# Kernel tuning notes

Hardware: AMD Instinct MI355X
Metric: run time of the kernel (lower is better)

## Reference

```python
import jax, jax.numpy as jnp
import numpy as np

L = 4        # num_blocks
D = 512      # d_model
H = 8        # num_heads
DFF = 2048   # d_ff
EPS = 1.1920929e-07  # torch RMSNorm default eps = finfo(fp32).eps


def setup_inputs() -> dict:
    key = jax.random.key(0)
    ks = jax.random.split(key, 12)
    B, S = 4, 1024
    s = 0.02
    return {
        "x": jax.random.normal(ks[0], (B, S, D), jnp.float32),
        "col_ids": jax.random.randint(ks[1], (B, S), 0, 32),
        "row_ids": jax.random.randint(ks[2], (B, S), 0, 128),
        "nbr_ids": jax.random.randint(ks[3], (B, S), 0, 64),
        # per-block, per-relation attention weights (nn.Linear: y = x @ W.T)
        "Wq": jax.random.normal(ks[4], (L, 4, D, D), jnp.float32) * s,
        "Wk": jax.random.normal(ks[5], (L, 4, D, D), jnp.float32) * s,
        "Wv": jax.random.normal(ks[6], (L, 4, D, D), jnp.float32) * s,
        "Wo": jax.random.normal(ks[7], (L, 4, D, D), jnp.float32) * s,
        # SwiGLU FFN weights per block
        "W1": jax.random.normal(ks[8], (L, DFF, D), jnp.float32) * s,
        "W3": jax.random.normal(ks[9], (L, DFF, D), jnp.float32) * s,
        "W2": jax.random.normal(ks[10], (L, D, DFF), jnp.float32) * s,
        # RMSNorm scales: 4 attn norms + 1 ffn norm per block + final norm_out
        "g_attn": jnp.ones((L, 4, D), jnp.float32),
        "g_ffn": jnp.ones((L, D), jnp.float32),
        "g_out": jnp.ones((D,), jnp.float32),
    }


def _rms(x, g):
    return x * jax.lax.rsqrt(jnp.mean(x * x, axis=-1, keepdims=True) + EPS) * g


def _attn(x, wq, wk, wv, wo, mask):
    # x: [B,S,D]; mask: [B,S,S] bool (True = attend) or None for full attention
    B, S, _ = x.shape
    hd = D // H
    scale = 1.0 / np.sqrt(hd).astype(np.float32)
    q = (x @ wq.T).reshape(B, S, H, hd).transpose(0, 2, 1, 3)  # bhsd
    k = (x @ wk.T).reshape(B, S, H, hd).transpose(0, 2, 1, 3)
    v = (x @ wv.T).reshape(B, S, H, hd).transpose(0, 2, 1, 3)
    sc = jnp.einsum('bhqd,bhkd->bhqk', q, k) * scale
    if mask is not None:
        sc = jnp.where(mask[:, None, :, :], sc, jnp.float32(-1e30))
    a = jax.nn.softmax(sc, axis=-1)
    o = jnp.einsum('bhqk,bhkd->bhqd', a, v).transpose(0, 2, 1, 3).reshape(B, S, D)
    return o @ wo.T


def reference(x, col_ids, row_ids, nbr_ids, Wq, Wk, Wv, Wo, W1, W3, W2, g_attn, g_ffn, g_out):
    # relation order in RelationalBlock: col, feat, nbr, full
    masks = [ids[:, :, None] == ids[:, None, :] for ids in (col_ids, row_ids, nbr_ids)] + [None]
    for l in range(L):
        for r in range(4):
            x = x + _attn(_rms(x, g_attn[l, r]), Wq[l, r], Wk[l, r], Wv[l, r], Wo[l, r], masks[r])
        h = _rms(x, g_ffn[l])
        x = x + (jax.nn.silu(h @ W1[l].T) * (h @ W3[l].T)) @ W2[l].T
    return _rms(x, g_out)
```

## Files before the change

kernel.cpp:

```cpp
#include <hip/hip_runtime.h>
#include <hip/hip_bf16.h>


typedef __attribute__((ext_vector_type(4))) float f32x4;
typedef __attribute__((ext_vector_type(8))) short s16x8;
typedef __attribute__((ext_vector_type(4))) short s16x4;
typedef __attribute__((ext_vector_type(16))) short s16x16;

#define SEQ 1024
#define DM 512
#define MTOT 4096
#define EPSV 1.1920929e-07f
#define LOG2E 1.44269504088896f

static __device__ __forceinline__ float b2f(short s) {
  unsigned u = ((unsigned)(unsigned short)s) << 16;
  return __builtin_bit_cast(float, u);
}
static __device__ __forceinline__ short f2b(float f) {
  unsigned u = __builtin_bit_cast(unsigned, f);
  u = (u + 0x7fffu + ((u >> 16) & 1u)) >> 16;
  return (short)(unsigned short)u;
}

#define MFMA_BF16(a, b, c) __builtin_amdgcn_mfma_f32_16x16x32_bf16((a), (b), (c), 0, 0, 0)
#define GLLDS(gp, lp)                                                                        \
  __builtin_amdgcn_global_load_lds((const __attribute__((address_space(1))) unsigned*)(gp),  \
                                   (__attribute__((address_space(3))) unsigned*)(lp), 16, 0, 0)
#define GLLDS4(gp, lp)                                                                       \
  __builtin_amdgcn_global_load_lds((const __attribute__((address_space(1))) unsigned*)(gp),  \
                                   (__attribute__((address_space(3))) unsigned*)(lp), 4, 0, 0)

__global__ void cvt_all(const f32x4* __restrict__ wq, const f32x4* __restrict__ wk,
                        const f32x4* __restrict__ wv, const f32x4* __restrict__ wo,
                        const f32x4* __restrict__ w1, const f32x4* __restrict__ w3,
                        const f32x4* __restrict__ w2, const float* __restrict__ g_attn,
                        const float* __restrict__ g_ffn, short* __restrict__ wqkv,
                        short* __restrict__ wob, short* __restrict__ w13,
                        short* __restrict__ w2b) {
  int i0 = (blockIdx.x * 256 + threadIdx.x) * 4;
  int which = blockIdx.y;
  s16x16 o;
  if (which < 3) {
    const f32x4* src = which == 0 ? wq : (which == 1 ? wk : wv);
    f32x4 v[4];
#pragma unroll
    for (int c = 0; c < 4; c++) v[c] = src[i0 + c];
    int lr = i0 >> 16, k4 = i0 & 127, n = (i0 >> 7) & 511;
    const float* gp = g_attn + lr * 512 + k4 * 4;
    float sc = (which == 0) ? 0.125f * LOG2E : 1.0f;
#pragma unroll
    for (int c = 0; c < 4; c++)
#pragma unroll
      for (int j = 0; j < 4; j++) o[c * 4 + j] = f2b(v[c][j] * gp[c * 4 + j] * sc);
    *(s16x16*)(wqkv + ((size_t)lr * 196608 + (which * 512 + n) * 128 + k4) * 4) = o;
  } else if (which == 3 || which == 6) {
    const f32x4* src = which == 3 ? wo : w2;
    short* dst = which == 3 ? wob : w2b;
    f32x4 v[4];
#pragma unroll
    for (int c = 0; c < 4; c++) v[c] = src[i0 + c];
#pragma unroll
    for (int c = 0; c < 4; c++)
#pragma unroll
      for (int j = 0; j < 4; j++) o[c * 4 + j] = f2b(v[c][j]);
    *(s16x16*)(dst + (size_t)i0 * 4) = o;
  } else {
    const f32x4* src = which == 4 ? w1 : w3;
    int off = which - 4;
    f32x4 v[4];
#pragma unroll
    for (int c = 0; c < 4; c++) v[c] = src[i0 + c];
    int l = i0 >> 18, n = (i0 >> 7) & 2047, k4 = i0 & 127;
    const float* gp = g_ffn + l * 512 + k4 * 4;
#pragma unroll
    for (int c = 0; c < 4; c++)
#pragma unroll
      for (int j = 0; j < 4; j++) o[c * 4 + j] = f2b(v[c][j] * gp[c * 4 + j]);
    *(s16x16*)(w13 + ((size_t)l * 524288 + (n * 2 + off) * 128 + k4) * 4) = o;
  }
}

__global__ void init_kernel(const float* __restrict__ xin, float* __restrict__ x,
                            short* __restrict__ h, float* __restrict__ sbuf) {
  int gid = blockIdx.x * 256 + threadIdx.x;
  if (gid < 20 * 4096) sbuf[4096 + gid] = 0.f;
  int row = blockIdx.x * 4 + (threadIdx.x >> 6);
  int lane = threadIdx.x & 63;
  const float* xr = xin + (size_t)row * DM + lane * 8;
  f32x4 a = *(const f32x4*)xr;
  f32x4 b = *(const f32x4*)(xr + 4);
  float* xo = x + (size_t)row * DM + lane * 8;
  *(f32x4*)xo = a;
  *(f32x4*)(xo + 4) = b;
  s16x8 ho;
#pragma unroll
  for (int j = 0; j < 4; j++) { ho[j] = f2b(a[j]); ho[4 + j] = f2b(b[j]); }
  *(s16x8*)(h + (size_t)row * DM + lane * 8) = ho;
  float ss = a[0]*a[0]+a[1]*a[1]+a[2]*a[2]+a[3]*a[3]+b[0]*b[0]+b[1]*b[1]+b[2]*b[2]+b[3]*b[3];
#pragma unroll
  for (int m = 1; m < 64; m <<= 1) ss += __shfl_xor(ss, m, 64);
  if (lane == 0) sbuf[row] = ss;
}

__global__ void rmsnorm_out(const float* __restrict__ x, const float* __restrict__ g,
                            float* __restrict__ outp) {
  int row = blockIdx.x * 4 + (threadIdx.x >> 6);
  int lane = threadIdx.x & 63;
  const float* xr = x + (size_t)row * DM + lane * 8;
  f32x4 a = *(const f32x4*)xr;
  f32x4 b = *(const f32x4*)(xr + 4);
  float ss = a[0]*a[0]+a[1]*a[1]+a[2]*a[2]+a[3]*a[3]+b[0]*b[0]+b[1]*b[1]+b[2]*b[2]+b[3]*b[3];
#pragma unroll
  for (int m = 1; m < 64; m <<= 1) ss += __shfl_xor(ss, m, 64);
  float sc = rsqrtf(ss * (1.0f / DM) + EPSV);
  const float* gp = g + lane * 8;
  float* o = outp + (size_t)row * DM + lane * 8;
  f32x4 o0, o1;
#pragma unroll
  for (int j = 0; j < 4; j++) { o0[j] = a[j] * sc * gp[j]; o1[j] = b[j] * sc * gp[4 + j]; }
  *(f32x4*)o = o0;
  *(f32x4*)(o + 4) = o1;
}

template<int AR, int AC, int FUSE>
__global__ __launch_bounds__(256) void gemm_bt(const short* __restrict__ A, const short* __restrict__ W,
                                               short* __restrict__ outb, float* __restrict__ outf,
                                               short* __restrict__ vtb,
                                               const float* __restrict__ ssq_in,
                                               float* __restrict__ ssq_out,
                                               short* __restrict__ hb, int N, int K) {
  constexpr int BM = AR * 32;
  constexpr int BN = AC * 32;
  constexpr int NA = BM / 64, NB = BN / 64;
  constexpr int LPS = NA + NB;
  __shared__ short As[2][BM * 32];
  __shared__ short Bs[2][BN * 32];
  const int tid = threadIdx.x;
  const int lane = tid & 63;
  const int w = tid >> 6;
  const int wr = w >> 1, wc = w & 1;
  const int qi = lane & 15, g = lane >> 4;
  const int m0 = blockIdx.x * BM, n0 = blockIdx.y * BN;

  const short* ap[NA];
  const short* wp[NB];
#pragma unroll
  for (int i = 0; i < NA; i++) {
    int s = i * 256 + tid;
    int row = s >> 2, gl = s & 3, gd = gl ^ ((row >> 1) & 3);
    ap[i] = A + (size_t)(m0 + row) * K + gd * 8;
  }
#pragma unroll
  for (int i = 0; i < NB; i++) {
    int s = i * 256 + tid;
    int row = s >> 2, gl = s & 3, gd = gl ^ ((row >> 1) & 3);
    wp[i] = W + (size_t)(n0 + row) * K + gd * 8;
  }
  int aro[AR], bro[AC];
#pragma unroll
  for (int i = 0; i < AR; i++) {
    int row = wr * AR * 16 + i * 16 + qi;
    aro[i] = row * 64 + ((g ^ ((row >> 1) & 3)) * 16);
  }
#pragma unroll
  for (int j = 0; j < AC; j++) {
    int row = wc * AC * 16 + j * 16 + qi;
    bro[j] = row * 64 + ((g ^ ((row >> 1) & 3)) * 16);
  }
  f32x4 acc[AR][AC] = {};

#define STAGE_G(BUF)                                                             \
  {                                                                              \
    _Pragma("unroll")                                                            \
    for (int i = 0; i < NA; i++) {                                               \
      GLLDS(ap[i], (char*)As[BUF] + (i * 256 + w * 64) * 16);                    \
      ap[i] += 32;                                                               \
    }                                                                            \
    _Pragma("unroll")                                                            \
    for (int i = 0; i < NB; i++) {                                               \
      GLLDS(wp[i], (char*)Bs[BUF] + (i * 256 + w * 64) * 16);                    \
      wp[i] += 32;                                                               \
    }                                                                            \
  }

#define BODY_G(BUF, T)                                                           \
  {                                                                              \
    s16x8 af[AR], bf[AC];                                                        \
    _Pragma("unroll")                                                            \
    for (int i = 0; i < AR; i++) af[i] = *(const s16x8*)((char*)As[BUF] + aro[i]); \
    _Pragma("unroll")                                                            \
    for (int j = 0; j < AC; j++) bf[j] = *(const s16x8*)((char*)Bs[BUF] + bro[j]); \
    asm volatile("s_waitcnt lgkmcnt(0)" ::: "memory");                           \
    __builtin_amdgcn_s_barrier();                                                \
    bool more = ((T) + 2 < nt);                                                  \
    if (more) STAGE_G(BUF);                                                      \
    _Pragma("unroll")                                                            \
    for (int i = 0; i < AR; i++)                                                 \
      _Pragma("unroll")                                                          \
      for (int j = 0; j < AC; j++)                                               \
        acc[i][j] = MFMA_BF16(af[i], bf[j], acc[i][j]);                          \
    if (more) asm volatile("s_waitcnt vmcnt(%0)" :: "n"(LPS) : "memory");        \
    else      asm volatile("s_waitcnt vmcnt(0)" ::: "memory");                   \
    __builtin_amdgcn_s_barrier();                                                \
  }

  const int nt = K >> 5;
  STAGE_G(0);
  STAGE_G(1);
  asm volatile("s_waitcnt vmcnt(%0)" :: "n"(LPS) : "memory");
  __builtin_amdgcn_s_barrier();
  for (int t = 0; t < nt; t += 2) {
    BODY_G(0, t);
    BODY_G(1, t + 1);
  }
#undef STAGE_G
#undef BODY_G

  float srow[AR][4];
  if (FUSE == 2 || FUSE == 3) {
#pragma unroll
    for (int i = 0; i < AR; i++) {
      int rbase = m0 + wr * AR * 16 + i * 16 + g * 4;
#pragma unroll
      for (int r = 0; r < 4; r++)
        srow[i][r] = rsqrtf(ssq_in[rbase + r] * (1.0f / DM) + EPSV);
    }
  }
  float part[AR][4];
  if (FUSE == 1) {
#pragma unroll
    for (int i = 0; i < AR; i++)
#pragma unroll
      for (int r = 0; r < 4; r++) part[i][r] = 0.f;
  }

#pragma unroll
  for (int i = 0; i < AR; i++) {
    int rbase = m0 + wr * AR * 16 + i * 16 + g * 4;
#pragma unroll
    for (int j = 0; j < AC; j++) {
      int col = n0 + wc * AC * 16 + j * 16 + qi;
      if (FUSE == 2 && col >= 1024) {
        int bbv = rbase >> 10, s = rbase & 1023;
        int c = col - 1024, hhv = c >> 6, d = c & 63;
        int o = (s & 63) >> 2;
        int gg = o & 3, h2 = (o >> 2) & 1, q32 = o >> 3;
        int pnew = q32 * 8 + gg * 2 + h2;
        s16x4 o4;
#pragma unroll
        for (int r = 0; r < 4; r++) o4[r] = f2b(acc[i][j][r] * srow[i][r]);
        *(s16x4*)(vtb + (((size_t)(bbv * 8 + hhv) * 64 + d) << 10) + (s & ~63) + pnew * 4) = o4;
      } else if (FUSE == 3) {
#pragma unroll
        for (int r = 0; r < 4; r++) {
          float own = acc[i][j][r] * srow[i][r];
          float other = __shfl_xor(own, 1, 64);
          float sv = own / (1.0f + __expf(-own));
          if (!(lane & 1))
            outb[(size_t)(rbase + r) * (N >> 1) + (col >> 1)] = f2b(sv * other);
        }
      } else if (FUSE == 1) {
#pragma unroll
        for (int r = 0; r < 4; r++) {
          size_t idx = (size_t)(rbase + r) * N + col;
          float xnew = outf[idx] + acc[i][j][r];
          outf[idx] = xnew;
          hb[idx] = f2b(xnew);
          part[i][r] += xnew * xnew;
        }
      } else {
#pragma unroll
        for (int r = 0; r < 4; r++)
          outb[(size_t)(rbase + r) * N + col] = f2b(acc[i][j][r] * srow[i][r]);
      }
    }
  }
  if (FUSE == 1) {
#pragma unroll
    for (int i = 0; i < AR; i++) {
      int rbase = m0 + wr * AR * 16 + i * 16 + g * 4;
#pragma unroll
      for (int r = 0; r < 4; r++) {
        float p = part[i][r];
#pragma unroll
        for (int m = 1; m < 16; m <<= 1) p += __shfl_xor(p, m, 16);
        if (qi == 0) atomicAdd(&ssq_out[rbase + r], p);
      }
    }
  }
}

__global__ __launch_bounds__(128) void attn_kernel(const short* __restrict__ qkv, const short* __restrict__ vt,
                                                   const int* __restrict__ ids, short* __restrict__ Ob) {
  const int bh = blockIdx.x;
  const int bb = bh >> 3, hh = bh & 7;
  const int q0 = blockIdx.y * 32;
  const int tid = threadIdx.x, lane = tid & 63, w = tid >> 6;
  const int g = lane >> 4, qi = lane & 15;
  __shared__ short Kl[2][64 * 64];
  __shared__ short Vl[2][64 * 64];
  __shared__ int Kid[2][64];
  const short* kbase = qkv + 512 + hh * 64;
  const short* vbase = vt + (size_t)bh * 64 * SEQ;
  s16x8 qf0, qf1;
  {
    int qrow = q0 + w * 16 + qi;
    const short* qp = qkv + (size_t)(bb * SEQ + qrow) * 1536 + hh * 64 + g * 8;
    qf0 = *(const s16x8*)qp;
    qf1 = *(const s16x8*)(qp + 32);
  }
  int qid = 0;
  if (ids) qid = ids[bb * SEQ + q0 + w * 16 + qi];
  float m_ = -1e30f, l_ = 0.f;
  f32x4 oacc[4] = {};

#define STAGE_ATTN(buf, ktt)                                                                     \
  {                                                                                              \
    _Pragma("unroll")                                                                            \
    for (int i = 0; i < 4; i++) {                                                                \
      int s = i * 128 + tid;                                                                     \
      int row = s >> 3, gl = s & 7, gd = gl ^ (row & 7);                                         \
      GLLDS(kbase + (size_t)(bb * SEQ + (ktt) + row) * 1536 + gd * 8,                            \
            (char*)Kl[buf] + (i * 128 + w * 64) * 16);                                           \
    }                                                                                            \
    _Pragma("unroll")                                                                            \
    for (int i = 0; i < 4; i++) {                                                                \
      int s = i * 128 + tid;                                                                     \
      int d = s >> 3, gl = s & 7, gd = gl ^ (d & 7);                                             \
      GLLDS(vbase + (size_t)d * SEQ + (ktt) + gd * 8, (char*)Vl[buf] + (i * 128 + w * 64) * 16); \
    }                                                                                            \
    if (ids && w == 0) GLLDS4(ids + bb * SEQ + (ktt) + lane, (char*)Kid[buf]);                   \
  }

  STAGE_ATTN(0, 0);
  __syncthreads();
  int cur = 0;
  for (int kt = 0; kt < SEQ; kt += 64) {
    if (kt + 64 < SEQ) STAGE_ATTN(cur ^ 1, kt + 64);
    f32x4 sc[4];
#pragma unroll
    for (int kc = 0; kc < 4; kc++) {
      int krow = kc * 16 + qi;
      s16x8 kf0 = *(const s16x8*)(Kl[cur] + krow * 64 + ((g ^ (krow & 7)) * 8));
      s16x8 kf1 = *(const s16x8*)(Kl[cur] + krow * 64 + (((4 + g) ^ (krow & 7)) * 8));
      f32x4 s4 = {};
      s4 = MFMA_BF16(kf0, qf0, s4);
      s4 = MFMA_BF16(kf1, qf1, s4);
      sc[kc] = s4;
    }
    float p[4][4];
#pragma unroll
    for (int kc = 0; kc < 4; kc++)
#pragma unroll
      for (int r = 0; r < 4; r++) p[kc][r] = sc[kc][r];
    if (ids) {
#pragma unroll
      for (int kc = 0; kc < 4; kc++) {
        int4 kid4 = *(const int4*)(Kid[cur] + kc * 16 + g * 4);
        if (kid4.x != qid) p[kc][0] = -1e30f;
        if (kid4.y != qid) p[kc][1] = -1e30f;
        if (kid4.z != qid) p[kc][2] = -1e30f;
        if (kid4.w != qid) p[kc][3] = -1e30f;
      }
    }
    float mx = fmaxf(fmaxf(p[0][0], p[0][1]), fmaxf(p[0][2], p[0][3]));
#pragma unroll
    for (int kc = 1; kc < 4; kc++)
      mx = fmaxf(mx, fmaxf(fmaxf(p[kc][0], p[kc][1]), fmaxf(p[kc][2], p[kc][3])));
    mx = fmaxf(mx, __shfl_xor(mx, 16, 64));
    mx = fmaxf(mx, __shfl_xor(mx, 32, 64));
    if (__any(mx > m_ + 8.f)) {
      float nm = fmaxf(m_, mx);
      float c = exp2f(m_ - nm);
      m_ = nm;
      l_ *= c;
#pragma unroll
      for (int r = 0; r < 4; r++) {
        float cr = __shfl(c, g * 4 + r, 16);
        oacc[0][r] *= cr; oacc[1][r] *= cr; oacc[2][r] *= cr; oacc[3][r] *= cr;
      }
    }
    float sum = 0.f;
#pragma unroll
    for (int kc = 0; kc < 4; kc++)
#pragma unroll
      for (int r = 0; r < 4; r++) {
        p[kc][r] = exp2f(p[kc][r] - m_);
        sum += p[kc][r];
      }
    sum += __shfl_xor(sum, 16, 64);
    sum += __shfl_xor(sum, 32, 64);
    l_ += sum;
    s16x8 pa, pb;
#pragma unroll
    for (int r = 0; r < 4; r++) {
      pa[r] = f2b(p[0][r]); pa[4 + r] = f2b(p[1][r]);
      pb[r] = f2b(p[2][r]); pb[4 + r] = f2b(p[3][r]);
    }
#pragma unroll
    for (int dt = 0; dt < 4; dt++) {
      int dl = dt * 16 + qi;
      const short* vr = Vl[cur] + dl * 64;
      s16x8 vf0 = *(const s16x8*)(vr + ((g ^ (dl & 7)) * 8));
      s16x8 vf1 = *(const s16x8*)(vr + (((4 + g) ^ (dl & 7)) * 8));
      oacc[dt] = MFMA_BF16(pa, vf0, oacc[dt]);
      oacc[dt] = MFMA_BF16(pb, vf1, oacc[dt]);
    }
    __syncthreads();
    cur ^= 1;
  }
#undef STAGE_ATTN
  const size_t obase = (size_t)(bb * SEQ) * DM + hh * 64;
#pragma unroll
  for (int r = 0; r < 4; r++) {
    float lr = __shfl(l_, g * 4 + r, 16);
    float inv = 1.0f / lr;
    int q = q0 + w * 16 + g * 4 + r;
#pragma unroll
    for (int dt = 0; dt < 4; dt++)
      Ob[obase + (size_t)q * DM + dt * 16 + qi] = f2b(oacc[dt][r] * inv);
  }
}

extern "C" void kernel_launch(void* const* d_in, const int* in_sizes, int n_in,
                              void* d_out, int out_size, void* d_ws, size_t ws_size,
                              hipStream_t stream) {
  const float* x_in  = (const float*)d_in[0];
  const int* col_ids = (const int*)d_in[1];
  const int* row_ids = (const int*)d_in[2];
  const int* nbr_ids = (const int*)d_in[3];
  const float* g_attn = (const float*)d_in[11];
  const float* g_ffn  = (const float*)d_in[12];
  const float* g_out  = (const float*)d_in[13];

  char* ws = (char*)d_ws;
  float* x    = (float*)(ws);
  short* h    = (short*)(ws + (size_t)(8u  << 20));
  short* qkv  = (short*)(ws + (size_t)(12u << 20));
  short* vt   = (short*)(ws + (size_t)(24u << 20));
  short* ob   = (short*)(ws + (size_t)(28u << 20));
  float* sbuf = (float*)(ws + (size_t)(33u << 20));
  short* fa   = (short*)(ws + (size_t)(44u << 20));
  short* wqkv = (short*)(ws + (size_t)(60u  << 20));
  short* wob  = (short*)(ws + (size_t)(84u  << 20));
  short* w13  = (short*)(ws + (size_t)(92u  << 20));
  short* w2b  = (short*)(ws + (size_t)(108u << 20));

  cvt_all<<<dim3(1024, 7), 256, 0, stream>>>((const f32x4*)d_in[4], (const f32x4*)d_in[5],
                                             (const f32x4*)d_in[6], (const f32x4*)d_in[7],
                                             (const f32x4*)d_in[8], (const f32x4*)d_in[9],
                                             (const f32x4*)d_in[10], g_attn, g_ffn,
                                             wqkv, wob, w13, w2b);
  init_kernel<<<1024, 256, 0, stream>>>(x_in, x, h, sbuf);

  const int* idsarr[4] = {col_ids, row_ids, nbr_ids, nullptr};

  for (int l = 0; l < 4; l++) {
    for (int r = 0; r < 4; r++) {
      int slot = l * 5 + r;
      size_t woff = (size_t)(l * 4 + r) * 1536 * DM;
      gemm_bt<4, 2, 2><<<dim3(32, 24), 256, 0, stream>>>(h, wqkv + woff, qkv, nullptr, vt,
                                                         sbuf + (size_t)slot * 4096, nullptr,
                                                         nullptr, 1536, DM);
      attn_kernel<<<dim3(32, 32), 128, 0, stream>>>(qkv, vt, idsarr[r], ob);
      gemm_bt<2, 2, 1><<<dim3(64, 8), 256, 0, stream>>>(ob, wob + (size_t)(l * 4 + r) * DM * DM,
                                                        nullptr, x, nullptr, nullptr,
                                                        sbuf + (size_t)(slot + 1) * 4096, h, DM, DM);
    }
    int fslot = l * 5 + 4;
    gemm_bt<4, 2, 3><<<dim3(32, 64), 256, 0, stream>>>(h, w13 + (size_t)l * 4096 * DM, fa, nullptr,
                                                       nullptr, sbuf + (size_t)fslot * 4096,
                                                       nullptr, nullptr, 4096, DM);
    gemm_bt<2, 2, 1><<<dim3(64, 8), 256, 0, stream>>>(fa, w2b + (size_t)l * DM * 2048, nullptr, x,
                                                      nullptr, nullptr,
                                                      sbuf + (size_t)(fslot + 1) * 4096, h, DM, 2048);
  }
  rmsnorm_out<<<1024, 256, 0, stream>>>(x, g_out, (float*)d_out);
}
```

Measured before the change: 1.214 ms.

## Sort tokens by relation id and skip key tiles outside each query group

Adds a counting-sort kernel that builds per-relation permutations grouping tokens with equal ids, plus per-position group start and end ranges. For the three masked relations, attention gathers queries and keys through the permutation and V is scattered into permuted order. Each query block then iterates only over the key range covering its groups, instead of all 1024 keys. The attention tile grows to 64 queries by 128 keys with 256 threads. The costs are indirect gathers, scalar scattered V stores and a serial rank loop in the sort. Skipping work depends on id groups being small, which holds for the test's random ids, but the mask stays exact for any ids.

```diff
diff --git a/kernel.cpp b/kernel.cpp
--- a/kernel.cpp
+++ b/kernel.cpp
@@ -30,6 +30,40 @@
 #define GLLDS4(gp, lp)                                                                       \
   __builtin_amdgcn_global_load_lds((const __attribute__((address_space(1))) unsigned*)(gp),  \
                                    (__attribute__((address_space(3))) unsigned*)(lp), 4, 0, 0)
+
+__global__ void sort_ids(const int* __restrict__ col, const int* __restrict__ row_,
+                         const int* __restrict__ nbr, int* __restrict__ perm,
+                         int* __restrict__ iperm, int* __restrict__ sid,
+                         int* __restrict__ rstart, int* __restrict__ rend) {
+  int r = blockIdx.x >> 2, b = blockIdx.x & 3;
+  const int* ids = (r == 0 ? col : (r == 1 ? row_ : nbr)) + b * SEQ;
+  int base = (r * 4 + b) * SEQ;
+  __shared__ int s_id[SEQ];
+  __shared__ int s_cnt[128];
+  __shared__ int s_pre[128];
+  int tid = threadIdx.x;
+  for (int i = tid; i < SEQ; i += 256) s_id[i] = ids[i];
+  if (tid < 128) s_cnt[tid] = 0;
+  __syncthreads();
+  for (int i = tid; i < SEQ; i += 256) atomicAdd(&s_cnt[s_id[i]], 1);
+  __syncthreads();
+  if (tid == 0) {
+    int acc = 0;
+    for (int v = 0; v < 128; v++) { s_pre[v] = acc; acc += s_cnt[v]; }
+  }
+  __syncthreads();
+  for (int i = tid; i < SEQ; i += 256) {
+    int id = s_id[i];
+    int rk = 0;
+    for (int j = 0; j < i; j++) rk += (s_id[j] == id);
+    int pos = s_pre[id] + rk;
+    perm[base + pos] = i;
+    iperm[base + i] = pos;
+    sid[base + pos] = id;
+    rstart[base + pos] = s_pre[id];
+    rend[base + pos] = s_pre[id] + s_cnt[id];
+  }
+}
 
 __global__ void cvt_all(const f32x4* __restrict__ wq, const f32x4* __restrict__ wk,
                         const f32x4* __restrict__ wv, const f32x4* __restrict__ wo,
@@ -129,7 +163,8 @@
                                                short* __restrict__ vtb,
                                                const float* __restrict__ ssq_in,
                                                float* __restrict__ ssq_out,
-                                               short* __restrict__ hb, int N, int K) {
+                                               short* __restrict__ hb,
+                                               const int* __restrict__ ipermt, int N, int K) {
   constexpr int BM = AR * 32;
   constexpr int BN = AC * 32;
   constexpr int NA = BM / 64, NB = BN / 64;
@@ -244,13 +279,25 @@
       if (FUSE == 2 && col >= 1024) {
         int bbv = rbase >> 10, s = rbase & 1023;
         int c = col - 1024, hhv = c >> 6, d = c & 63;
-        int o = (s & 63) >> 2;
-        int gg = o & 3, h2 = (o >> 2) & 1, q32 = o >> 3;
-        int pnew = q32 * 8 + gg * 2 + h2;
-        s16x4 o4;
-#pragma unroll
-        for (int r = 0; r < 4; r++) o4[r] = f2b(acc[i][j][r] * srow[i][r]);
-        *(s16x4*)(vtb + (((size_t)(bbv * 8 + hhv) * 64 + d) << 10) + (s & ~63) + pnew * 4) = o4;
+        size_t vrowbase = ((size_t)(bbv * 8 + hhv) * 64 + d) << 10;
+        if (ipermt) {
+#pragma unroll
+          for (int r = 0; r < 4; r++) {
+            int pos = ipermt[bbv * 1024 + s + r];
+            int o = (pos & 63) >> 2;
+            int pnew = (o >> 3) * 8 + (o & 3) * 2 + ((o >> 2) & 1);
+            int dp = (pos & ~63) + pnew * 4 + (pos & 3);
+            vtb[vrowbase + dp] = f2b(acc[i][j][r] * srow[i][r]);
+          }
+        } else {
+          int o = (s & 63) >> 2;
+          int gg = o & 3, h2 = (o >> 2) & 1, q32 = o >> 3;
+          int pnew = q32 * 8 + gg * 2 + h2;
+          s16x4 o4;
+#pragma unroll
+          for (int r = 0; r < 4; r++) o4[r] = f2b(acc[i][j][r] * srow[i][r]);
+          *(s16x4*)(vtb + vrowbase + (s & ~63) + pnew * 4) = o4;
+        }
       } else if (FUSE == 3) {
 #pragma unroll
         for (int r = 0; r < 4; r++) {
@@ -291,27 +338,35 @@
   }
 }
 
-__global__ __launch_bounds__(128) void attn_kernel(const short* __restrict__ qkv, const short* __restrict__ vt,
-                                                   const int* __restrict__ ids, short* __restrict__ Ob) {
+__global__ __launch_bounds__(256) void attn_kernel(const short* __restrict__ qkv, const short* __restrict__ vt,
+                                                   const int* __restrict__ sidt, const int* __restrict__ permt,
+                                                   const int* __restrict__ rst, const int* __restrict__ ret,
+                                                   short* __restrict__ Ob) {
   const int bh = blockIdx.x;
   const int bb = bh >> 3, hh = bh & 7;
-  const int q0 = blockIdx.y * 32;
+  const int q0 = blockIdx.y * 64;
   const int tid = threadIdx.x, lane = tid & 63, w = tid >> 6;
   const int g = lane >> 4, qi = lane & 15;
-  __shared__ short Kl[2][64 * 64];
-  __shared__ short Vl[2][64 * 64];
-  __shared__ int Kid[2][64];
+  __shared__ short Kl[2][128 * 64];
+  __shared__ short Vl[2][64 * 128];
+  __shared__ int Kid[2][128];
   const short* kbase = qkv + 512 + hh * 64;
   const short* vbase = vt + (size_t)bh * 64 * SEQ;
   s16x8 qf0, qf1;
   {
-    int qrow = q0 + w * 16 + qi;
+    int qp_ = q0 + w * 16 + qi;
+    int qrow = permt ? permt[bb * SEQ + qp_] : qp_;
     const short* qp = qkv + (size_t)(bb * SEQ + qrow) * 1536 + hh * 64 + g * 8;
     qf0 = *(const s16x8*)qp;
     qf1 = *(const s16x8*)(qp + 32);
   }
   int qid = 0;
-  if (ids) qid = ids[bb * SEQ + q0 + w * 16 + qi];
+  if (permt) qid = sidt[bb * SEQ + q0 + w * 16 + qi];
+  int kt0 = 0, kend = SEQ;
+  if (permt) {
+    kt0 = rst[bb * SEQ + q0] & ~127;
+    kend = ret[bb * SEQ + q0 + 63];
+  }
   float m_ = -1e30f, l_ = 0.f;
   f32x4 oacc[4] = {};
 
@@ -319,28 +374,30 @@
   {                                                                                              \
     _Pragma("unroll")                                                                            \
     for (int i = 0; i < 4; i++) {                                                                \
-      int s = i * 128 + tid;                                                                     \
+      int s = i * 256 + tid;                                                                     \
       int row = s >> 3, gl = s & 7, gd = gl ^ (row & 7);                                         \
-      GLLDS(kbase + (size_t)(bb * SEQ + (ktt) + row) * 1536 + gd * 8,                            \
-            (char*)Kl[buf] + (i * 128 + w * 64) * 16);                                           \
+      int krow = (ktt) + row;                                                                    \
+      int kr = permt ? permt[bb * SEQ + krow] : krow;                                            \
+      GLLDS(kbase + (size_t)(bb * SEQ + kr) * 1536 + gd * 8,                                     \
+            (char*)Kl[buf] + (i * 256 + w * 64) * 16);                                           \
     }                                                                                            \
     _Pragma("unroll")                                                                            \
     for (int i = 0; i < 4; i++) {                                                                \
-      int s = i * 128 + tid;                                                                     \
-      int d = s >> 3, gl = s & 7, gd = gl ^ (d & 7);                                             \
-      GLLDS(vbase + (size_t)d * SEQ + (ktt) + gd * 8, (char*)Vl[buf] + (i * 128 + w * 64) * 16); \
+      int s = i * 256 + tid;                                                                     \
+      int d = s >> 4, gl = s & 15, gd = gl ^ (d & 7);                                            \
+      GLLDS(vbase + (size_t)d * SEQ + (ktt) + gd * 8, (char*)Vl[buf] + (i * 256 + w * 64) * 16); \
     }                                                                                            \
-    if (ids && w == 0) GLLDS4(ids + bb * SEQ + (ktt) + lane, (char*)Kid[buf]);                   \
-  }
-
-  STAGE_ATTN(0, 0);
+    if (permt && w < 2) GLLDS4(sidt + bb * SEQ + (ktt) + w * 64 + lane, (char*)Kid[buf] + w * 256); \
+  }
+
+  STAGE_ATTN(0, kt0);
   __syncthreads();
   int cur = 0;
-  for (int kt = 0; kt < SEQ; kt += 64) {
-    if (kt + 64 < SEQ) STAGE_ATTN(cur ^ 1, kt + 64);
-    f32x4 sc[4];
-#pragma unroll
-    for (int kc = 0; kc < 4; kc++) {
+  for (int kt = kt0; kt < kend; kt += 128) {
+    if (kt + 128 < kend) STAGE_ATTN(cur ^ 1, kt + 128);
+    f32x4 sc[8];
+#pragma unroll
+    for (int kc = 0; kc < 8; kc++) {
       int krow = kc * 16 + qi;
       s16x8 kf0 = *(const s16x8*)(Kl[cur] + krow * 64 + ((g ^ (krow & 7)) * 8));
       s16x8 kf1 = *(const s16x8*)(Kl[cur] + krow * 64 + (((4 + g) ^ (krow & 7)) * 8));
@@ -349,14 +406,14 @@
       s4 = MFMA_BF16(kf1, qf1, s4);
       sc[kc] = s4;
     }
-    float p[4][4];
-#pragma unroll
-    for (int kc = 0; kc < 4; kc++)
+    float p[8][4];
+#pragma unroll
+    for (int kc = 0; kc < 8; kc++)
 #pragma unroll
       for (int r = 0; r < 4; r++) p[kc][r] = sc[kc][r];
-    if (ids) {
-#pragma unroll
-      for (int kc = 0; kc < 4; kc++) {
+    if (permt) {
+#pragma unroll
+      for (int kc = 0; kc < 8; kc++) {
         int4 kid4 = *(const int4*)(Kid[cur] + kc * 16 + g * 4);
         if (kid4.x != qid) p[kc][0] = -1e30f;
         if (kid4.y != qid) p[kc][1] = -1e30f;
@@ -366,7 +423,7 @@
     }
     float mx = fmaxf(fmaxf(p[0][0], p[0][1]), fmaxf(p[0][2], p[0][3]));
 #pragma unroll
-    for (int kc = 1; kc < 4; kc++)
+    for (int kc = 1; kc < 8; kc++)
       mx = fmaxf(mx, fmaxf(fmaxf(p[kc][0], p[kc][1]), fmaxf(p[kc][2], p[kc][3])));
     mx = fmaxf(mx, __shfl_xor(mx, 16, 64));
     mx = fmaxf(mx, __shfl_xor(mx, 32, 64));
@@ -383,7 +440,7 @@
     }
     float sum = 0.f;
 #pragma unroll
-    for (int kc = 0; kc < 4; kc++)
+    for (int kc = 0; kc < 8; kc++)
 #pragma unroll
       for (int r = 0; r < 4; r++) {
         p[kc][r] = exp2f(p[kc][r] - m_);
@@ -392,20 +449,23 @@
     sum += __shfl_xor(sum, 16, 64);
     sum += __shfl_xor(sum, 32, 64);
     l_ += sum;
-    s16x8 pa, pb;
-#pragma unroll
-    for (int r = 0; r < 4; r++) {
-      pa[r] = f2b(p[0][r]); pa[4 + r] = f2b(p[1][r]);
-      pb[r] = f2b(p[2][r]); pb[4 + r] = f2b(p[3][r]);
-    }
-#pragma unroll
-    for (int dt = 0; dt < 4; dt++) {
-      int dl = dt * 16 + qi;
-      const short* vr = Vl[cur] + dl * 64;
-      s16x8 vf0 = *(const s16x8*)(vr + ((g ^ (dl & 7)) * 8));
-      s16x8 vf1 = *(const s16x8*)(vr + (((4 + g) ^ (dl & 7)) * 8));
-      oacc[dt] = MFMA_BF16(pa, vf0, oacc[dt]);
-      oacc[dt] = MFMA_BF16(pb, vf1, oacc[dt]);
+#pragma unroll
+    for (int kk = 0; kk < 2; kk++) {
+      s16x8 pa, pb;
+#pragma unroll
+      for (int r = 0; r < 4; r++) {
+        pa[r] = f2b(p[kk * 4 + 0][r]); pa[4 + r] = f2b(p[kk * 4 + 1][r]);
+        pb[r] = f2b(p[kk * 4 + 2][r]); pb[4 + r] = f2b(p[kk * 4 + 3][r]);
+      }
+#pragma unroll
+      for (int dt = 0; dt < 4; dt++) {
+        int dl = dt * 16 + qi;
+        const short* vr = Vl[cur] + dl * 128;
+        s16x8 vf0 = *(const s16x8*)(vr + (kk * 8 + (g ^ (dl & 7))) * 8);
+        s16x8 vf1 = *(const s16x8*)(vr + (kk * 8 + ((4 + g) ^ (dl & 7))) * 8);
+        oacc[dt] = MFMA_BF16(pa, vf0, oacc[dt]);
+        oacc[dt] = MFMA_BF16(pb, vf1, oacc[dt]);
+      }
     }
     __syncthreads();
     cur ^= 1;
@@ -416,7 +476,8 @@
   for (int r = 0; r < 4; r++) {
     float lr = __shfl(l_, g * 4 + r, 16);
     float inv = 1.0f / lr;
-    int q = q0 + w * 16 + g * 4 + r;
+    int qp_ = q0 + w * 16 + g * 4 + r;
+    int q = permt ? permt[bb * SEQ + qp_] : qp_;
 #pragma unroll
     for (int dt = 0; dt < 4; dt++)
       Ob[obase + (size_t)q * DM + dt * 16 + qi] = f2b(oacc[dt][r] * inv);
@@ -441,12 +502,20 @@
   short* vt   = (short*)(ws + (size_t)(24u << 20));
   short* ob   = (short*)(ws + (size_t)(28u << 20));
   float* sbuf = (float*)(ws + (size_t)(33u << 20));
+  int*   ptab = (int*)(ws + (size_t)(35u << 20));
   short* fa   = (short*)(ws + (size_t)(44u << 20));
   short* wqkv = (short*)(ws + (size_t)(60u  << 20));
   short* wob  = (short*)(ws + (size_t)(84u  << 20));
   short* w13  = (short*)(ws + (size_t)(92u  << 20));
   short* w2b  = (short*)(ws + (size_t)(108u << 20));
 
+  int* perm  = ptab;
+  int* iperm = ptab + 12288;
+  int* sid   = ptab + 24576;
+  int* rst   = ptab + 36864;
+  int* ret   = ptab + 49152;
+
+  sort_ids<<<12, 256, 0, stream>>>(col_ids, row_ids, nbr_ids, perm, iperm, sid, rst, ret);
   cvt_all<<<dim3(1024, 7), 256, 0, stream>>>((const f32x4*)d_in[4], (const f32x4*)d_in[5],
                                              (const f32x4*)d_in[6], (const f32x4*)d_in[7],
                                              (const f32x4*)d_in[8], (const f32x4*)d_in[9],
@@ -454,27 +523,32 @@
                                              wqkv, wob, w13, w2b);
   init_kernel<<<1024, 256, 0, stream>>>(x_in, x, h, sbuf);
 
-  const int* idsarr[4] = {col_ids, row_ids, nbr_ids, nullptr};
-
   for (int l = 0; l < 4; l++) {
     for (int r = 0; r < 4; r++) {
       int slot = l * 5 + r;
       size_t woff = (size_t)(l * 4 + r) * 1536 * DM;
+      const int* ip = (r < 3) ? iperm + r * 4096 : nullptr;
       gemm_bt<4, 2, 2><<<dim3(32, 24), 256, 0, stream>>>(h, wqkv + woff, qkv, nullptr, vt,
                                                          sbuf + (size_t)slot * 4096, nullptr,
-                                                         nullptr, 1536, DM);
-      attn_kernel<<<dim3(32, 32), 128, 0, stream>>>(qkv, vt, idsarr[r], ob);
+                                                         nullptr, ip, 1536, DM);
+      if (r < 3)
+        attn_kernel<<<dim3(32, 16), 256, 0, stream>>>(qkv, vt, sid + r * 4096, perm + r * 4096,
+                                                      rst + r * 4096, ret + r * 4096, ob);
+      else
+        attn_kernel<<<dim3(32, 16), 256, 0, stream>>>(qkv, vt, nullptr, nullptr, nullptr, nullptr, ob);
       gemm_bt<2, 2, 1><<<dim3(64, 8), 256, 0, stream>>>(ob, wob + (size_t)(l * 4 + r) * DM * DM,
                                                         nullptr, x, nullptr, nullptr,
-                                                        sbuf + (size_t)(slot + 1) * 4096, h, DM, DM);
+                                                        sbuf + (size_t)(slot + 1) * 4096, h,
+                                                        nullptr, DM, DM);
     }
     int fslot = l * 5 + 4;
     gemm_bt<4, 2, 3><<<dim3(32, 64), 256, 0, stream>>>(h, w13 + (size_t)l * 4096 * DM, fa, nullptr,
                                                        nullptr, sbuf + (size_t)fslot * 4096,
-                                                       nullptr, nullptr, 4096, DM);
+                                                       nullptr, nullptr, nullptr, 4096, DM);
     gemm_bt<2, 2, 1><<<dim3(64, 8), 256, 0, stream>>>(fa, w2b + (size_t)l * DM * 2048, nullptr, x,
                                                       nullptr, nullptr,
-                                                      sbuf + (size_t)(fslot + 1) * 4096, h, DM, 2048);
+                                                      sbuf + (size_t)(fslot + 1) * 4096, h,
+                                                      nullptr, DM, 2048);
   }
   rmsnorm_out<<<1024, 256, 0, stream>>>(x, g_out, (float*)d_out);
 }
```

Result: slower. 1.257 ms (+3.5%).
